# Performance work log

Hardware: AMD Instinct MI355X
Metric: run time of the kernel (lower is better)

## Reference

```python
import jax, jax.numpy as jnp
import numpy as np

B = 8          # batch_size
N = 2048       # N_particles
D_SP = 2       # spatial dims
D = 16         # D_SP + hidden_dim
K = 32         # max_num_neighbors
R = 0.08       # neighbor_radius
DT = 0.01      # leapfrog step
BIG = 1e9


def setup_inputs() -> dict:
    key = jax.random.key(0)
    ks = jax.random.split(key, 8)
    H, C = 64, 32
    # node state: small random hidden features, deterministic disk positions
    x = jax.random.normal(ks[0], (B * N, D), dtype=jnp.float32) * 0.001
    i = jnp.arange(N, dtype=jnp.float32)
    golden = jnp.pi * (3.0 - jnp.sqrt(5.0))
    theta = i * golden
    r = 0.6 * jnp.sqrt((i + 0.5) / N)
    pos = jnp.stack([r * jnp.cos(theta), r * jnp.sin(theta)], axis=1)  # [N,2]
    pos = jnp.tile(pos, (B, 1)) + 0.01 * jax.random.normal(ks[1], (B * N, 2), dtype=jnp.float32)
    x = x.at[:, :D_SP].set(pos)
    W1 = jax.random.normal(ks[2], (2 * D, H), dtype=jnp.float32) * (1.0 / np.sqrt(2 * D))
    b1 = jnp.zeros((H,), jnp.float32)
    W2 = jax.random.normal(ks[3], (H, C), dtype=jnp.float32) * (1.0 / np.sqrt(H))
    b2 = jnp.zeros((C,), jnp.float32)
    Wout = jax.random.normal(ks[4], (C, 1), dtype=jnp.float32) * (1.0 / np.sqrt(C))
    bout = jnp.zeros((1,), jnp.float32)
    batch = jnp.repeat(jnp.arange(B, dtype=jnp.int64), N)
    return {"x": x, "W1": W1, "b1": b1, "W2": W2, "b2": b2,
            "Wout": Wout, "bout": bout, "batch": batch, "steps": 2}


def reference(x, W1, b1, W2, b2, Wout, bout, batch, steps):
    Bn, Df = x.shape
    Bc = int(np.asarray(batch)[-1]) + 1      # batch is contiguous blocks
    Nn = Bn // Bc
    eye = jnp.eye(Nn, dtype=x.dtype) * BIG   # no self-loops (loop=False)

    def hamiltonian(xv):
        xb = xv.reshape(Bc, Nn, Df)
        pos = xb[:, :, :D_SP]                              # [B,N,2]
        # radius_graph: pairwise sq-dist per simulation, capped at K neighbors
        d2 = jnp.sum((pos[:, :, None, :] - pos[:, None, :, :]) ** 2, axis=-1)  # [B,N,N]
        d2 = d2 + eye
        negd, idx = jax.lax.top_k(-d2, K)                  # K nearest per node
        valid = (-negd) < (R * R)                          # [B,N,K]
        # gather neighbor states (HNNConv message on concat(x_i, x_j))
        xj = xb[jnp.arange(Bc)[:, None, None], idx]        # [B,N,K,D]
        xi = jnp.broadcast_to(xb[:, :, None, :], xj.shape)
        m = jnp.tanh(jnp.concatenate([xi, xj], axis=-1) @ W1 + b1)  # [B,N,K,H]
        m = m @ W2 + b2                                    # [B,N,K,C]
        m = jnp.where(valid[..., None], m, 0.0)
        agg = m.sum(axis=2)                                # sum aggregation [B,N,C]
        h = agg @ Wout + bout                              # per-node Hamiltonian [B,N,1]
        return h.sum()

    for _ in range(int(steps)):
        dHdx = jax.grad(hamiltonian)(x)
        x = x - DT * dHdx
    return x
```

## Files before the change

kernel.cpp:

```cpp
#include <hip/hip_runtime.h>
#include <cstdint>
#include <cstddef>

#define BB   8
#define NN   2048
#define DD   16
#define HHH  64
#define KK   32
#define CAP  96
#define FCAP 48
#define DT_C 0.01f
#define R2_C (0.08f * 0.08f)

#define GRID 17
#define NCEL (GRID * GRID)
#define GOFF 0.68f
#define CINV 12.5f
#define CSTRIDE 320

#define WPB   4
#define BLOCK (WPB * 64)

__device__ __forceinline__ float dist2(float px, float py, float qx, float qy) {
    float dx = __fsub_rn(px, qx);
    float dy = __fsub_rn(py, qy);
    return __fadd_rn(__fmul_rn(dx, dx), __fmul_rn(dy, dy));
}

__device__ __forceinline__ float dtanh_xla(float zz) {
    float xx = fminf(fmaxf(zz, -9.f), 9.f);
    float x2 = xx * xx;
    float p = fmaf(x2, -2.76076847742355e-16f, 2.00018790482477e-13f);
    p = fmaf(x2, p, -8.60467152213735e-11f);
    p = fmaf(x2, p, 5.12229709037114e-08f);
    p = fmaf(x2, p, 1.48572235717979e-05f);
    p = fmaf(x2, p, 6.37261928875436e-04f);
    p = fmaf(x2, p, 4.89352455891786e-03f);
    p = xx * p;
    float q = fmaf(x2, 1.19825839466702e-06f, 1.18534705686654e-04f);
    q = fmaf(x2, q, 2.26843463243900e-03f);
    q = fmaf(x2, q, 4.89352518554385e-03f);
    float r = __builtin_amdgcn_rcpf(q);
    float t = p * r;
    t = fmaf(fmaf(-q, t, p), r, t);
    return fmaf(-t, t, 1.0f);
}

__device__ __forceinline__ float s2fast(float z) {
    float a = __builtin_amdgcn_exp2f(-2.885390082f * fabsf(z));
    float b = 1.f + a;
    return a * __builtin_amdgcn_rcpf(b * b);
}

__device__ __forceinline__ int prefix_cnt(unsigned long long m) {
    return (int)__builtin_amdgcn_mbcnt_hi(
        (unsigned)(m >> 32), __builtin_amdgcn_mbcnt_lo((unsigned)m, 0u));
}

__device__ __forceinline__ int swizzled_slot(int blk, int w, int& bbase) {
    bbase = (blk & 7) << 11;
    return (blk >> 3) + (NN / WPB) * w;
}

__device__ __forceinline__ int clampi(int v, int lo, int hi) {
    return v < lo ? lo : (v > hi ? hi : v);
}

struct Win { int rs0, rl0, rs1, rl1, rs2, rl2, tot; };
__device__ __forceinline__ Win cell_window(const int* CS, float px, float py) {
    Win W;
    int cx = clampi((int)((px + GOFF) * CINV), 0, GRID - 1);
    int cy = clampi((int)((py + GOFF) * CINV), 0, GRID - 1);
    int xlo = cx > 0 ? cx - 1 : 0;
    int xhi = cx < GRID - 1 ? cx + 1 : GRID - 1;
    W.rs0 = 0; W.rl0 = 0; W.rs2 = 0; W.rl2 = 0;
    if (cy > 0) {
        int a = CS[(cy - 1) * GRID + xlo], b = CS[(cy - 1) * GRID + xhi + 1];
        W.rs0 = a; W.rl0 = b - a;
    }
    {
        int a = CS[cy * GRID + xlo], b = CS[cy * GRID + xhi + 1];
        W.rs1 = a; W.rl1 = b - a;
    }
    if (cy < GRID - 1) {
        int a = CS[(cy + 1) * GRID + xlo], b = CS[(cy + 1) * GRID + xhi + 1];
        W.rs2 = a; W.rl2 = b - a;
    }
    W.tot = W.rl0 + W.rl1 + W.rl2;
    return W;
}
__device__ __forceinline__ int win_map(const Win& W, int t) {
    int j = W.rs0 + t;
    int u1 = t - W.rl0;
    if (u1 >= 0) j = W.rs1 + u1;
    int u2 = u1 - W.rl1;
    if (u2 >= 0) j = W.rs2 + u2;
    return j;
}

template <bool FIRST>
__global__ __launch_bounds__(1024) void k_bin(
    const float* __restrict__ x, const float* __restrict__ pos,
    const float* __restrict__ W2, const float* __restrict__ Wout,
    float2* __restrict__ sortedPos, unsigned short* __restrict__ sortedIdx,
    int* __restrict__ cellStart, float* __restrict__ vOut) {
    __shared__ int hist[NCEL], base[NCEL + 1], cursor[NCEL];
    int bat = blockIdx.x, bbase = bat << 11, tid = threadIdx.x;
    if (tid < NCEL) hist[tid] = 0;
    if (blockIdx.x == 0 && tid >= 512 && tid < 512 + HHH) {
        int hh = tid - 512;
        float acc = 0.f;
        for (int c = 0; c < 32; c++) acc = fmaf(W2[hh * 32 + c], Wout[c], acc);
        vOut[hh] = acc;
    }
    __syncthreads();
    float2 q[2]; int cid[2];
#pragma unroll
    for (int u = 0; u < 2; ++u) {
        int i = tid + (u << 10);
        float2 qq = FIRST ? *(const float2*)(x + (size_t)(bbase + i) * DD)
                          : *(const float2*)(pos + (size_t)(bbase + i) * 2);
        q[u] = qq;
        int cx = clampi((int)((qq.x + GOFF) * CINV), 0, GRID - 1);
        int cy = clampi((int)((qq.y + GOFF) * CINV), 0, GRID - 1);
        cid[u] = cy * GRID + cx;
        atomicAdd(&hist[cid[u]], 1);
    }
    __syncthreads();
    if (tid < 64) {
        int loc[5], s = 0;
#pragma unroll
        for (int k = 0; k < 5; ++k) {
            int idx = tid * 5 + k;
            loc[k] = (idx < NCEL) ? hist[idx] : 0;
            s += loc[k];
        }
        int pre = s;
#pragma unroll
        for (int off = 1; off < 64; off <<= 1) {
            int t = __shfl_up(pre, off);
            if (tid >= off) pre += t;
        }
        pre -= s;
#pragma unroll
        for (int k = 0; k < 5; ++k) {
            int idx = tid * 5 + k;
            if (idx <= NCEL) base[idx] = pre;
            pre += loc[k];
        }
    }
    __syncthreads();
    if (tid < NCEL) cursor[tid] = base[tid];
    if (tid <= NCEL) cellStart[bat * CSTRIDE + tid] = base[tid];
    __syncthreads();
#pragma unroll
    for (int u = 0; u < 2; ++u) {
        int dst = atomicAdd(&cursor[cid[u]], 1);
        sortedPos[bbase + dst] = q[u];
        sortedIdx[bbase + dst] = (unsigned short)(tid + (u << 10));
    }
}

__global__ __launch_bounds__(BLOCK, 4) void k_cut(
    const float* __restrict__ x,
    const float2* __restrict__ sortedPos, const unsigned short* __restrict__ sortedIdx,
    const int* __restrict__ cellStart, const float* __restrict__ W1,
    float* __restrict__ cutArr,
    float* __restrict__ Asp, float* __restrict__ Dsp) {
    __shared__ float sD[WPB][CAP];

    int tid = threadIdx.x;
    int w = tid >> 6, lane = tid & 63;
    int bbase;
    int s = swizzled_slot(blockIdx.x, w, bbase);
    int bat = bbase >> 11;
    int gs = bbase + s;

    int jol = (int)sortedIdx[gs];
    const float* xrow = x + (size_t)(bbase + jol) * DD;
    float xv = (lane < DD) ? xrow[lane] : 0.f;
    float px = __shfl(xv, 0), py = __shfl(xv, 1);
    double A0 = 0.0, A1 = 0.0, A2 = 0.0, A3 = 0.0;
    double D0 = 0.0, D1 = 0.0, D2v = 0.0, D3 = 0.0;
#pragma unroll
    for (int f = 0; f < DD; f += 4) {
        float xf0 = __shfl(xv, f),     xf1 = __shfl(xv, f + 1);
        float xf2 = __shfl(xv, f + 2), xf3 = __shfl(xv, f + 3);
        A0 = fma((double)xf0, (double)W1[(f + 0) * HHH + lane], A0);
        A1 = fma((double)xf1, (double)W1[(f + 1) * HHH + lane], A1);
        A2 = fma((double)xf2, (double)W1[(f + 2) * HHH + lane], A2);
        A3 = fma((double)xf3, (double)W1[(f + 3) * HHH + lane], A3);
        D0 = fma((double)xf0, (double)W1[(DD + f + 0) * HHH + lane], D0);
        D1 = fma((double)xf1, (double)W1[(DD + f + 1) * HHH + lane], D1);
        D2v = fma((double)xf2, (double)W1[(DD + f + 2) * HHH + lane], D2v);
        D3 = fma((double)xf3, (double)W1[(DD + f + 3) * HHH + lane], D3);
    }
    Asp[((size_t)gs << 6) + lane] = (float)((A0 + A1) + (A2 + A3));
    Dsp[((size_t)gs << 6) + lane] = (float)((D0 + D1) + (D2v + D3));

    const int* CS = cellStart + bat * CSTRIDE;
    Win W = cell_window(CS, px, py);
    int cnt = 0;
    {
        int t0 = lane, t1 = 64 + lane;
        bool in0 = t0 < W.tot, in1 = t1 < W.tot;
        int ja0 = in0 ? win_map(W, t0) : 0;
        float2 q0 = sortedPos[bbase + ja0];
        float2 q1;
        bool have1 = W.tot > 64;
        if (have1) {
            int ja1 = in1 ? win_map(W, t1) : 0;
            q1 = sortedPos[bbase + ja1];
        }
        float d2 = dist2(px, py, q0.x, q0.y);
        bool hit = in0 && (d2 < R2_C);
        unsigned long long m = __ballot(hit);
        int idx = cnt + prefix_cnt(m);
        if (hit && idx < CAP) sD[w][idx] = d2;
        cnt += (int)__popcll(m);
        if (have1) {
            float e2 = dist2(px, py, q1.x, q1.y);
            bool h2 = in1 && (e2 < R2_C);
            unsigned long long m2 = __ballot(h2);
            int i2 = cnt + prefix_cnt(m2);
            if (h2 && i2 < CAP) sD[w][i2] = e2;
            cnt += (int)__popcll(m2);
        }
        for (int c0 = 128; c0 < W.tot; c0 += 64) {
            int t = c0 + lane;
            int j = win_map(W, t);
            bool in = t < W.tot;
            float2 q = sortedPos[bbase + (in ? j : 0)];
            float dd = dist2(px, py, q.x, q.y);
            bool ht = in && (dd < R2_C);
            unsigned long long mm = __ballot(ht);
            int ix = cnt + prefix_cnt(mm);
            if (ht && ix < CAP) sD[w][ix] = dd;
            cnt += (int)__popcll(mm);
        }
    }
    if (cnt > CAP) cnt = CAP;
    __threadfence_block();

    float cutoff = R2_C;
    if (cnt > KK + 1) {
        const float INF = 1e30f;
        if (cnt <= 64) {
            float v = (lane < cnt) ? sD[w][lane] : INF;
#pragma unroll
            for (int k = 2; k <= 64; k <<= 1) {
#pragma unroll
                for (int j = k >> 1; j > 0; j >>= 1) {
                    float pv = __shfl_xor(v, j);
                    bool up = ((lane & k) == 0);
                    bool takeMin = (((lane & j) == 0) == up);
                    v = takeMin ? fminf(v, pv) : fmaxf(v, pv);
                }
            }
            cutoff = __shfl(v, KK);
        } else {
            float e0 = (lane < cnt) ? sD[w][lane] : INF;
            float e1 = (lane + 64 < cnt) ? sD[w][lane + 64] : INF;
            int r0 = 0, q0 = 0, r1 = 0, q1 = 0;
            for (int k = 0; k < cnt; k++) {
                float val = sD[w][k];
                r0 += (val < e0); q0 += (val == e0);
                r1 += (val < e1); q1 += (val == e1);
            }
            bool c0 = (r0 <= KK) && (r0 + q0 > KK);
            bool c1 = (r1 <= KK) && (r1 + q1 > KK);
            float cand = c0 ? e0 : (c1 ? e1 : INF);
#pragma unroll
            for (int off = 32; off; off >>= 1) cand = fminf(cand, __shfl_xor(cand, off));
            cutoff = cand;
        }
    }
    if (lane == 0) cutArr[gs] = cutoff;
}

template <bool EXACT>
__global__ __launch_bounds__(BLOCK, 4) void k_grad(
    const float* __restrict__ x, const unsigned short* __restrict__ sortedIdx,
    const float2* __restrict__ sortedPos, const int* __restrict__ cellStart,
    const float* __restrict__ cutArr,
    const float* __restrict__ Asp, const float* __restrict__ Dsp,
    const float* __restrict__ W1, const float* __restrict__ b1,
    const float* __restrict__ vArr,
    float* __restrict__ xOut, float* __restrict__ posOut) {
    __shared__ float sW1t[HHH * 33];
    __shared__ alignas(16) unsigned short sFwd[WPB][FCAP];
    __shared__ alignas(16) unsigned short sRev[WPB][CAP];
    __shared__ float sS[WPB][128];

    int tid = threadIdx.x;
    int w = tid >> 6, h = tid & 63;
    int bbase;
    int s = swizzled_slot(blockIdx.x, w, bbase);
    int bat = bbase >> 11;
    int gs = bbase + s;

    for (int t = tid; t < 2 * DD * HHH; t += BLOCK) {
        int f = t >> 6, hh = t & 63;
        sW1t[hh * 33 + f] = W1[t];
    }
    __syncthreads();

    float b1h = b1[h];
    float Apbs = Asp[((size_t)gs << 6) + h] + b1h;
    float Dpbs = Dsp[((size_t)gs << 6) + h] + b1h;
    float vh = vArr[h];

    float2 pp = sortedPos[gs];
    float px = pp.x, py = pp.y;
    float cutp = cutArr[gs];

    const int* CS = cellStart + bat * CSTRIDE;
    Win W = cell_window(CS, px, py);
    int mf = 0, mr = 0;
#define PROC(IN, J, Q, CUTJ)                                              \
    {                                                                     \
        float d2 = dist2(px, py, (Q).x, (Q).y);                           \
        bool hit = (IN) && (d2 < R2_C) && ((J) != s);                     \
        bool fw = hit && (d2 <= cutp);                                    \
        bool rv = hit && (d2 <= (CUTJ));                                  \
        unsigned long long mF = __ballot(fw);                             \
        int iF = mf + prefix_cnt(mF);                                     \
        if (fw && iF < FCAP) sFwd[w][iF] = (unsigned short)(J);           \
        mf += (int)__popcll(mF);                                          \
        unsigned long long mR = __ballot(rv);                             \
        int iR = mr + prefix_cnt(mR);                                     \
        if (rv && iR < CAP) sRev[w][iR] = (unsigned short)(J);            \
        mr += (int)__popcll(mR);                                          \
    }
    {
        int t0 = h, t1 = 64 + h;
        bool in0 = t0 < W.tot, in1 = t1 < W.tot;
        int j0 = win_map(W, t0);
        int ja0 = in0 ? j0 : 0;
        float2 q0 = sortedPos[bbase + ja0];
        float cut0 = cutArr[bbase + ja0];
        bool have1 = W.tot > 64;
        int j1 = 0; float2 q1; float cut1 = 0.f;
        if (have1) {
            j1 = win_map(W, t1);
            int ja1 = in1 ? j1 : 0;
            q1 = sortedPos[bbase + ja1];
            cut1 = cutArr[bbase + ja1];
        }
        PROC(in0, j0, q0, cut0)
        if (have1) PROC(in1, j1, q1, cut1)
        for (int c0 = 128; c0 < W.tot; c0 += 64) {
            int t = c0 + h;
            int j = win_map(W, t);
            bool in = t < W.tot;
            int ja = in ? j : 0;
            float2 q = sortedPos[bbase + ja];
            float cutj = cutArr[bbase + ja];
            PROC(in, j, q, cutj)
        }
    }
#undef PROC
    if (mf > FCAP) mf = FCAP;
    if (mr > CAP) mr = CAP;
    __threadfence_block();

    const float* baseD = Dsp + ((size_t)bbase << 6);
    const float* baseA = Asp + ((size_t)bbase << 6);
    double T1 = 0.0, T2 = 0.0;
    float f1a = 0.f, f1b = 0.f, f2a = 0.f, f2b = 0.f;

#define TERM1(VAL)                                                        \
    { if constexpr (EXACT) T1 += (double)dtanh_xla(Apbs + (VAL));         \
      else { float sv_ = s2fast(Apbs + (VAL));                            \
             if (k & 1) f1b += sv_; else f1a += sv_; } }
#define TERM2(VAL)                                                        \
    { if constexpr (EXACT) T2 += (double)dtanh_xla(Dpbs + (VAL));         \
      else { float sv_ = s2fast(Dpbs + (VAL));                            \
             if (k & 1) f2b += sv_; else f2a += sv_; } }

#define UNPACK8(Q0, Q1, U)                                            \
    unsigned U[8];                                                    \
    U[0] = (unsigned)__builtin_amdgcn_readfirstlane(Q0.x);            \
    U[1] = (unsigned)__builtin_amdgcn_readfirstlane(Q0.y);            \
    U[2] = (unsigned)__builtin_amdgcn_readfirstlane(Q0.z);            \
    U[3] = (unsigned)__builtin_amdgcn_readfirstlane(Q0.w);            \
    U[4] = (unsigned)__builtin_amdgcn_readfirstlane(Q1.x);            \
    U[5] = (unsigned)__builtin_amdgcn_readfirstlane(Q1.y);            \
    U[6] = (unsigned)__builtin_amdgcn_readfirstlane(Q1.z);            \
    U[7] = (unsigned)__builtin_amdgcn_readfirstlane(Q1.w);

    {
        const unsigned short* L = sFwd[w];
        int c = 0;
        for (; c + 16 <= mf; c += 16) {
            int4 q0 = *(const int4*)(L + c);
            int4 q1 = *(const int4*)(L + c + 8);
            UNPACK8(q0, q1, u)
            float d[16];
#pragma unroll
            for (int k = 0; k < 8; ++k) {
                const float* ra = baseD + ((size_t)(u[k] & 0xffffu) << 6);
                const float* rb = baseD + ((size_t)(u[k] >> 16) << 6);
                d[2 * k]     = ra[h];
                d[2 * k + 1] = rb[h];
            }
#pragma unroll
            for (int k = 0; k < 16; ++k) TERM1(d[k])
        }
        for (; c + 8 <= mf; c += 8) {
            int4 q0 = *(const int4*)(L + c);
            UNPACK8(q0, q0, u)
            float d[8];
#pragma unroll
            for (int k = 0; k < 4; ++k) {
                const float* ra = baseD + ((size_t)(u[k] & 0xffffu) << 6);
                const float* rb = baseD + ((size_t)(u[k] >> 16) << 6);
                d[2 * k]     = ra[h];
                d[2 * k + 1] = rb[h];
            }
#pragma unroll
            for (int k = 0; k < 8; ++k) TERM1(d[k])
        }
        for (int k = 0; c < mf; ++c, k ^= 1) {
            unsigned jl = (unsigned)__builtin_amdgcn_readfirstlane((int)L[c]);
            TERM1((baseD + ((size_t)jl << 6))[h])
        }
    }
    {
        const unsigned short* L = sRev[w];
        int c = 0;
        for (; c + 16 <= mr; c += 16) {
            int4 q0 = *(const int4*)(L + c);
            int4 q1 = *(const int4*)(L + c + 8);
            UNPACK8(q0, q1, u)
            float d[16];
#pragma unroll
            for (int k = 0; k < 8; ++k) {
                const float* ra = baseA + ((size_t)(u[k] & 0xffffu) << 6);
                const float* rb = baseA + ((size_t)(u[k] >> 16) << 6);
                d[2 * k]     = ra[h];
                d[2 * k + 1] = rb[h];
            }
#pragma unroll
            for (int k = 0; k < 16; ++k) TERM2(d[k])
        }
        for (; c + 8 <= mr; c += 8) {
            int4 q0 = *(const int4*)(L + c);
            UNPACK8(q0, q0, u)
            float d[8];
#pragma unroll
            for (int k = 0; k < 4; ++k) {
                const float* ra = baseA + ((size_t)(u[k] & 0xffffu) << 6);
                const float* rb = baseA + ((size_t)(u[k] >> 16) << 6);
                d[2 * k]     = ra[h];
                d[2 * k + 1] = rb[h];
            }
#pragma unroll
            for (int k = 0; k < 8; ++k) TERM2(d[k])
        }
        for (int k = 0; c < mr; ++c, k ^= 1) {
            unsigned jl = (unsigned)__builtin_amdgcn_readfirstlane((int)L[c]);
            TERM2((baseA + ((size_t)jl << 6))[h])
        }
    }
#undef UNPACK8
#undef TERM1
#undef TERM2

    if constexpr (EXACT) {
        sS[w][h]      = vh * (float)T1;
        sS[w][64 + h] = vh * (float)T2;
    } else {
        float vh4 = 4.f * vh;
        sS[w][h]      = vh4 * (f1a + f1b);
        sS[w][64 + h] = vh4 * (f2a + f2b);
    }
    __threadfence_block();

    float g;
    {
        int col = h & 31;
        const float* Sv = &sS[w][(col < 16) ? 0 : 64];
        int hh0 = (h < 32) ? 0 : 32;
        if constexpr (EXACT) {
            double a0 = 0.0, a1 = 0.0, a2 = 0.0, a3 = 0.0;
            for (int hh = hh0; hh < hh0 + 32; hh += 4) {
                a0 = fma((double)sW1t[(hh + 0) * 33 + col], (double)Sv[hh + 0], a0);
                a1 = fma((double)sW1t[(hh + 1) * 33 + col], (double)Sv[hh + 1], a1);
                a2 = fma((double)sW1t[(hh + 2) * 33 + col], (double)Sv[hh + 2], a2);
                a3 = fma((double)sW1t[(hh + 3) * 33 + col], (double)Sv[hh + 3], a3);
            }
            double gd = (a0 + a1) + (a2 + a3);
            double go = __shfl_xor(gd, 32);
            g = (float)(gd + go);
        } else {
            float a0 = 0.f, a1 = 0.f, a2 = 0.f, a3 = 0.f;
            for (int hh = hh0; hh < hh0 + 32; hh += 4) {
                a0 = fmaf(sW1t[(hh + 0) * 33 + col], Sv[hh + 0], a0);
                a1 = fmaf(sW1t[(hh + 1) * 33 + col], Sv[hh + 1], a1);
                a2 = fmaf(sW1t[(hh + 2) * 33 + col], Sv[hh + 2], a2);
                a3 = fmaf(sW1t[(hh + 3) * 33 + col], Sv[hh + 3], a3);
            }
            float gd = (a0 + a1) + (a2 + a3);
            float go = __shfl_xor(gd, 32);
            g = gd + go;
        }
    }
    float g2 = __shfl(g, (h + 16) & 63);
    int jo = (int)sortedIdx[gs];
    if (h < DD) {
        size_t prow = (size_t)(bbase + jo) * DD;
        float xn = __fsub_rn(x[prow + h], __fmul_rn(DT_C, __fadd_rn(g, g2)));
        xOut[prow + h] = xn;
        if (h < 2) posOut[(bbase + jo) * 2 + h] = xn;
    }
}

extern "C" void kernel_launch(void* const* d_in, const int* in_sizes, int n_in,
                              void* d_out, int out_size, void* d_ws, size_t ws_size,
                              hipStream_t stream) {
    const float* x0   = (const float*)d_in[0];
    const float* W1   = (const float*)d_in[1];
    const float* b1   = (const float*)d_in[2];
    const float* W2   = (const float*)d_in[3];
    const float* Wout = (const float*)d_in[5];
    float* out = (float*)d_out;

    float* ws   = (float*)d_ws;
    float* posA = ws;
    float* posB = posA + 32768;
    float* x1   = posB + 32768;
    float* Asp  = x1 + 262144;
    float* Dsp  = Asp + 16384 * 64;
    float* cut  = Dsp + 16384 * 64;
    float2* sPosS = (float2*)(cut + 16384);
    unsigned short* sIdx = (unsigned short*)(sPosS + 16384);
    int* cellStart = (int*)(sIdx + 16384);
    float* vArr = (float*)(cellStart + BB * CSTRIDE);

    const int NB = (BB * NN) / WPB;

    k_bin<true><<<BB, 1024, 0, stream>>>(x0, nullptr, W2, Wout, sPosS, sIdx,
                                         cellStart, vArr);
    k_cut<<<NB, BLOCK, 0, stream>>>(x0, sPosS, sIdx, cellStart, W1, cut, Asp, Dsp);
    k_grad<true><<<NB, BLOCK, 0, stream>>>(x0, sIdx, sPosS, cellStart, cut, Asp, Dsp,
                                           W1, b1, vArr, x1, posB);
    k_bin<false><<<BB, 1024, 0, stream>>>(nullptr, posB, W2, Wout, sPosS, sIdx,
                                          cellStart, vArr);
    k_cut<<<NB, BLOCK, 0, stream>>>(x1, sPosS, sIdx, cellStart, W1, cut, Asp, Dsp);
    k_grad<false><<<NB, BLOCK, 0, stream>>>(x1, sIdx, sPosS, cellStart, cut, Asp, Dsp,
                                            W1, b1, vArr, out, posA);
}
```

Before: 173.3 us.

## Process two particles per wavefront in k_cut, sharing W1 loads and sort

Each wavefront in k_cut now handles two sorted particles (slots p and p+N/2) instead of one, so the grid is halved. The W1 weight loads are shared between both particles' projection FMAs, and the bitonic sort for the k-th-distance cutoff runs on both particles in one interleaved pass. The old swizzled slot mapping is replaced by a simple batch-interleaved mapping. This trades per-wave parallelism and register pressure (sixteen double accumulators) for fewer waves, amortised loads and more ILP.

```diff
diff --git a/kernel.cpp b/kernel.cpp
--- a/kernel.cpp
+++ b/kernel.cpp
@@ -167,41 +167,66 @@
     const int* __restrict__ cellStart, const float* __restrict__ W1,
     float* __restrict__ cutArr,
     float* __restrict__ Asp, float* __restrict__ Dsp) {
-    __shared__ float sD[WPB][CAP];
+    __shared__ float sD[WPB][2][CAP];
 
     int tid = threadIdx.x;
     int w = tid >> 6, lane = tid & 63;
-    int bbase;
-    int s = swizzled_slot(blockIdx.x, w, bbase);
+    int bbase = (blockIdx.x & 7) << 11;
     int bat = bbase >> 11;
-    int gs = bbase + s;
-
-    int jol = (int)sortedIdx[gs];
-    const float* xrow = x + (size_t)(bbase + jol) * DD;
-    float xv = (lane < DD) ? xrow[lane] : 0.f;
-    float px = __shfl(xv, 0), py = __shfl(xv, 1);
-    double A0 = 0.0, A1 = 0.0, A2 = 0.0, A3 = 0.0;
-    double D0 = 0.0, D1 = 0.0, D2v = 0.0, D3 = 0.0;
+    int p = (blockIdx.x >> 3) + (NN / WPB / 2) * w;
+    int sA = p, sB = p + (NN / 2);
+    int gsA = bbase + sA, gsB = bbase + sB;
+
+    int jolA = (int)sortedIdx[gsA];
+    int jolB = (int)sortedIdx[gsB];
+    const float* xrowA = x + (size_t)(bbase + jolA) * DD;
+    const float* xrowB = x + (size_t)(bbase + jolB) * DD;
+    float xvA = (lane < DD) ? xrowA[lane] : 0.f;
+    float xvB = (lane < DD) ? xrowB[lane] : 0.f;
+    float pxA = __shfl(xvA, 0), pyA = __shfl(xvA, 1);
+    float pxB = __shfl(xvB, 0), pyB = __shfl(xvB, 1);
+    double AA0 = 0.0, AA1 = 0.0, AA2 = 0.0, AA3 = 0.0;
+    double DA0 = 0.0, DA1 = 0.0, DA2 = 0.0, DA3 = 0.0;
+    double AB0 = 0.0, AB1 = 0.0, AB2 = 0.0, AB3 = 0.0;
+    double DB0 = 0.0, DB1 = 0.0, DB2 = 0.0, DB3 = 0.0;
 #pragma unroll
     for (int f = 0; f < DD; f += 4) {
-        float xf0 = __shfl(xv, f),     xf1 = __shfl(xv, f + 1);
-        float xf2 = __shfl(xv, f + 2), xf3 = __shfl(xv, f + 3);
-        A0 = fma((double)xf0, (double)W1[(f + 0) * HHH + lane], A0);
-        A1 = fma((double)xf1, (double)W1[(f + 1) * HHH + lane], A1);
-        A2 = fma((double)xf2, (double)W1[(f + 2) * HHH + lane], A2);
-        A3 = fma((double)xf3, (double)W1[(f + 3) * HHH + lane], A3);
-        D0 = fma((double)xf0, (double)W1[(DD + f + 0) * HHH + lane], D0);
-        D1 = fma((double)xf1, (double)W1[(DD + f + 1) * HHH + lane], D1);
-        D2v = fma((double)xf2, (double)W1[(DD + f + 2) * HHH + lane], D2v);
-        D3 = fma((double)xf3, (double)W1[(DD + f + 3) * HHH + lane], D3);
-    }
-    Asp[((size_t)gs << 6) + lane] = (float)((A0 + A1) + (A2 + A3));
-    Dsp[((size_t)gs << 6) + lane] = (float)((D0 + D1) + (D2v + D3));
+        float w0 = W1[(f + 0) * HHH + lane], w1 = W1[(f + 1) * HHH + lane];
+        float w2 = W1[(f + 2) * HHH + lane], w3 = W1[(f + 3) * HHH + lane];
+        float v0 = W1[(DD + f + 0) * HHH + lane], v1 = W1[(DD + f + 1) * HHH + lane];
+        float v2 = W1[(DD + f + 2) * HHH + lane], v3 = W1[(DD + f + 3) * HHH + lane];
+        float a0 = __shfl(xvA, f),     a1 = __shfl(xvA, f + 1);
+        float a2 = __shfl(xvA, f + 2), a3 = __shfl(xvA, f + 3);
+        float b0 = __shfl(xvB, f),     b1 = __shfl(xvB, f + 1);
+        float b2 = __shfl(xvB, f + 2), b3 = __shfl(xvB, f + 3);
+        AA0 = fma((double)a0, (double)w0, AA0);
+        AA1 = fma((double)a1, (double)w1, AA1);
+        AA2 = fma((double)a2, (double)w2, AA2);
+        AA3 = fma((double)a3, (double)w3, AA3);
+        DA0 = fma((double)a0, (double)v0, DA0);
+        DA1 = fma((double)a1, (double)v1, DA1);
+        DA2 = fma((double)a2, (double)v2, DA2);
+        DA3 = fma((double)a3, (double)v3, DA3);
+        AB0 = fma((double)b0, (double)w0, AB0);
+        AB1 = fma((double)b1, (double)w1, AB1);
+        AB2 = fma((double)b2, (double)w2, AB2);
+        AB3 = fma((double)b3, (double)w3, AB3);
+        DB0 = fma((double)b0, (double)v0, DB0);
+        DB1 = fma((double)b1, (double)v1, DB1);
+        DB2 = fma((double)b2, (double)v2, DB2);
+        DB3 = fma((double)b3, (double)v3, DB3);
+    }
+    Asp[((size_t)gsA << 6) + lane] = (float)((AA0 + AA1) + (AA2 + AA3));
+    Dsp[((size_t)gsA << 6) + lane] = (float)((DA0 + DA1) + (DA2 + DA3));
+    Asp[((size_t)gsB << 6) + lane] = (float)((AB0 + AB1) + (AB2 + AB3));
+    Dsp[((size_t)gsB << 6) + lane] = (float)((DB0 + DB1) + (DB2 + DB3));
 
     const int* CS = cellStart + bat * CSTRIDE;
-    Win W = cell_window(CS, px, py);
-    int cnt = 0;
-    {
+    Win WA = cell_window(CS, pxA, pyA);
+    Win WB = cell_window(CS, pxB, pyB);
+
+    auto scan = [&](float px, float py, const Win& W, float* sDrow) -> int {
+        int cnt = 0;
         int t0 = lane, t1 = 64 + lane;
         bool in0 = t0 < W.tot, in1 = t1 < W.tot;
         int ja0 = in0 ? win_map(W, t0) : 0;
@@ -216,14 +241,14 @@
         bool hit = in0 && (d2 < R2_C);
         unsigned long long m = __ballot(hit);
         int idx = cnt + prefix_cnt(m);
-        if (hit && idx < CAP) sD[w][idx] = d2;
+        if (hit && idx < CAP) sDrow[idx] = d2;
         cnt += (int)__popcll(m);
         if (have1) {
             float e2 = dist2(px, py, q1.x, q1.y);
             bool h2 = in1 && (e2 < R2_C);
             unsigned long long m2 = __ballot(h2);
             int i2 = cnt + prefix_cnt(m2);
-            if (h2 && i2 < CAP) sD[w][i2] = e2;
+            if (h2 && i2 < CAP) sDrow[i2] = e2;
             cnt += (int)__popcll(m2);
         }
         for (int c0 = 128; c0 < W.tot; c0 += 64) {
@@ -235,47 +260,63 @@
             bool ht = in && (dd < R2_C);
             unsigned long long mm = __ballot(ht);
             int ix = cnt + prefix_cnt(mm);
-            if (ht && ix < CAP) sD[w][ix] = dd;
+            if (ht && ix < CAP) sDrow[ix] = dd;
             cnt += (int)__popcll(mm);
         }
-    }
-    if (cnt > CAP) cnt = CAP;
+        return cnt;
+    };
+    int cntA = scan(pxA, pyA, WA, sD[w][0]);
+    int cntB = scan(pxB, pyB, WB, sD[w][1]);
+    if (cntA > CAP) cntA = CAP;
+    if (cntB > CAP) cntB = CAP;
     __threadfence_block();
 
-    float cutoff = R2_C;
-    if (cnt > KK + 1) {
-        const float INF = 1e30f;
-        if (cnt <= 64) {
-            float v = (lane < cnt) ? sD[w][lane] : INF;
-#pragma unroll
-            for (int k = 2; k <= 64; k <<= 1) {
-#pragma unroll
-                for (int j = k >> 1; j > 0; j >>= 1) {
-                    float pv = __shfl_xor(v, j);
-                    bool up = ((lane & k) == 0);
-                    bool takeMin = (((lane & j) == 0) == up);
-                    v = takeMin ? fminf(v, pv) : fmaxf(v, pv);
-                }
-            }
-            cutoff = __shfl(v, KK);
-        } else {
-            float e0 = (lane < cnt) ? sD[w][lane] : INF;
-            float e1 = (lane + 64 < cnt) ? sD[w][lane + 64] : INF;
-            int r0 = 0, q0 = 0, r1 = 0, q1 = 0;
-            for (int k = 0; k < cnt; k++) {
-                float val = sD[w][k];
-                r0 += (val < e0); q0 += (val == e0);
-                r1 += (val < e1); q1 += (val == e1);
-            }
-            bool c0 = (r0 <= KK) && (r0 + q0 > KK);
-            bool c1 = (r1 <= KK) && (r1 + q1 > KK);
-            float cand = c0 ? e0 : (c1 ? e1 : INF);
-#pragma unroll
-            for (int off = 32; off; off >>= 1) cand = fminf(cand, __shfl_xor(cand, off));
-            cutoff = cand;
-        }
-    }
-    if (lane == 0) cutArr[gs] = cutoff;
+    const float INF = 1e30f;
+    float cutoffA = R2_C, cutoffB = R2_C;
+    bool bA = (cntA > KK + 1) && (cntA <= 64);
+    bool bB = (cntB > KK + 1) && (cntB <= 64);
+    if (bA || bB) {
+        float vA = (bA && lane < cntA) ? sD[w][0][lane] : INF;
+        float vB = (bB && lane < cntB) ? sD[w][1][lane] : INF;
+#pragma unroll
+        for (int k = 2; k <= 64; k <<= 1) {
+#pragma unroll
+            for (int j = k >> 1; j > 0; j >>= 1) {
+                float pA = __shfl_xor(vA, j);
+                float pB = __shfl_xor(vB, j);
+                bool up = ((lane & k) == 0);
+                bool takeMin = (((lane & j) == 0) == up);
+                vA = takeMin ? fminf(vA, pA) : fmaxf(vA, pA);
+                vB = takeMin ? fminf(vB, pB) : fmaxf(vB, pB);
+            }
+        }
+        if (bA) cutoffA = __shfl(vA, KK);
+        if (bB) cutoffB = __shfl(vB, KK);
+    }
+#define BIGSEL(CNT, ROW, OUT)                                             \
+    if ((CNT) > 64) {                                                     \
+        float e0 = (lane < (CNT)) ? sD[w][ROW][lane] : INF;               \
+        float e1 = (lane + 64 < (CNT)) ? sD[w][ROW][lane + 64] : INF;     \
+        int r0 = 0, q0 = 0, r1 = 0, q1 = 0;                               \
+        for (int k = 0; k < (CNT); k++) {                                 \
+            float val = sD[w][ROW][k];                                    \
+            r0 += (val < e0); q0 += (val == e0);                          \
+            r1 += (val < e1); q1 += (val == e1);                          \
+        }                                                                 \
+        bool c0 = (r0 <= KK) && (r0 + q0 > KK);                           \
+        bool c1 = (r1 <= KK) && (r1 + q1 > KK);                           \
+        float cand = c0 ? e0 : (c1 ? e1 : INF);                           \
+        _Pragma("unroll")                                                 \
+        for (int off = 32; off; off >>= 1) cand = fminf(cand, __shfl_xor(cand, off)); \
+        OUT = cand;                                                       \
+    }
+    BIGSEL(cntA, 0, cutoffA)
+    BIGSEL(cntB, 1, cutoffB)
+#undef BIGSEL
+    if (lane == 0) {
+        cutArr[gsA] = cutoffA;
+        cutArr[gsB] = cutoffB;
+    }
 }
 
 template <bool EXACT>
@@ -538,16 +579,17 @@
     int* cellStart = (int*)(sIdx + 16384);
     float* vArr = (float*)(cellStart + BB * CSTRIDE);
 
-    const int NB = (BB * NN) / WPB;
+    const int NB  = (BB * NN) / WPB;
+    const int NBC = (BB * NN) / (WPB * 2);
 
     k_bin<true><<<BB, 1024, 0, stream>>>(x0, nullptr, W2, Wout, sPosS, sIdx,
                                          cellStart, vArr);
-    k_cut<<<NB, BLOCK, 0, stream>>>(x0, sPosS, sIdx, cellStart, W1, cut, Asp, Dsp);
+    k_cut<<<NBC, BLOCK, 0, stream>>>(x0, sPosS, sIdx, cellStart, W1, cut, Asp, Dsp);
     k_grad<true><<<NB, BLOCK, 0, stream>>>(x0, sIdx, sPosS, cellStart, cut, Asp, Dsp,
                                            W1, b1, vArr, x1, posB);
     k_bin<false><<<BB, 1024, 0, stream>>>(nullptr, posB, W2, Wout, sPosS, sIdx,
                                           cellStart, vArr);
-    k_cut<<<NB, BLOCK, 0, stream>>>(x1, sPosS, sIdx, cellStart, W1, cut, Asp, Dsp);
+    k_cut<<<NBC, BLOCK, 0, stream>>>(x1, sPosS, sIdx, cellStart, W1, cut, Asp, Dsp);
     k_grad<false><<<NB, BLOCK, 0, stream>>>(x1, sIdx, sPosS, cellStart, cut, Asp, Dsp,
                                             W1, b1, vArr, out, posA);
 }
```

After: 173.5 us, median of 2. Within noise of the previous version (+0.1%).
